# Kernel tuning notes

Hardware: AMD Instinct MI355X
Metric: run time of the kernel (lower is better)

The kernel has to match this reference:

```python
import jax, jax.numpy as jnp
import numpy as np

L = 4          # num_layers
H = 128        # hidden_channels
F = 128        # num_filters
G = 25         # num_gaussians
N = 10000      # nodes
E = 320000     # radius-graph edges
EH = 40000     # hull edges
NG = 64        # graphs in batch
CUTOFF = 5.0
PI = float(np.pi)
LOG2 = float(np.log(2.0))


def ssp(x):  # ShiftedSoftplus
    return jax.nn.softplus(x) - LOG2


def setup_inputs() -> dict:
    key = jax.random.key(0)
    ks = iter(jax.random.split(key, 64))
    w = lambda shape: jax.random.normal(next(ks), shape, jnp.float32) * 0.05
    inp = {
        'z': jax.random.randint(next(ks), (N,), 0, 100),
        'edge_index': jax.random.randint(next(ks), (2, E), 0, N),
        'edge_index_hull': jax.random.randint(next(ks), (2, EH), 0, N),
        'batch': jnp.sort(jax.random.randint(next(ks), (N,), 0, NG)),
        'dist': jax.random.uniform(next(ks), (E,), jnp.float32) * CUTOFF,
        'fea_hull': jax.random.normal(next(ks), (EH, 7), jnp.float32),
        'emb_table': w((100, H)),
        'lin_w': w((L, F, H)),
        'mlp_w1': w((L, F, G)), 'mlp_b1': jnp.zeros((L, F), jnp.float32),
        'mlp_w2': w((L, F, F)), 'mlp_b2': jnp.zeros((L, F), jnp.float32),
        'linh_w': w((L, F, H)),
        'mlph_w1': w((L, F, 7)), 'mlph_b1': jnp.zeros((L, F), jnp.float32),
        'mlph_w2': w((L, F, F)), 'mlph_b2': jnp.zeros((L, F), jnp.float32),
        'v1_w': w((L, H, F)), 'v1_b': jnp.zeros((L, H), jnp.float32),
        'v2_w': w((L, 64, H)), 'v2_b': jnp.zeros((L, 64), jnp.float32),
        'vh1_w': w((L, H, F)), 'vh1_b': jnp.zeros((L, H), jnp.float32),
        'vh2_w': w((L, 64, H)), 'vh2_b': jnp.zeros((L, 64), jnp.float32),
        'cat_w': w((L, H, 128)), 'cat_b': jnp.zeros((L, H), jnp.float32),
        'u1_w': w((64, H)), 'u1_b': jnp.zeros((64,), jnp.float32),
        'u2_w': w((1, 64)), 'u2_b': jnp.zeros((1,), jnp.float32),
    }
    return inp


def reference(z, edge_index, edge_index_hull, batch, dist, fea_hull, emb_table,
              lin_w, mlp_w1, mlp_b1, mlp_w2, mlp_b2,
              linh_w, mlph_w1, mlph_b1, mlph_w2, mlph_b2,
              v1_w, v1_b, v2_w, v2_b, vh1_w, vh1_b, vh2_w, vh2_b,
              cat_w, cat_b, u1_w, u1_b, u2_w, u2_b):
    n = z.shape[0]
    # Gaussian distance embedding: emb(0, cutoff, G)
    offset = jnp.linspace(0.0, CUTOFF, G)
    coeff = -0.5 / (offset[1] - offset[0]) ** 2
    dist_emb = jnp.exp(coeff * (dist[:, None] - offset[None, :]) ** 2)  # [E,G]
    C = 0.5 * (jnp.cos(dist * PI / CUTOFF) + 1.0)                       # [E]
    j, i = edge_index[0], edge_index[1]
    jh, ih = edge_index_hull[0], edge_index_hull[1]
    v = emb_table[z]                                                    # [N,H]
    for l in range(L):
        # update_e
        W = (ssp(dist_emb @ mlp_w1[l].T + mlp_b1[l]) @ mlp_w2[l].T + mlp_b2[l]) * C[:, None]
        e = (v @ lin_w[l].T)[j] * W                                     # [E,F]
        Wh = ssp(fea_hull @ mlph_w1[l].T + mlph_b1[l]) @ mlph_w2[l].T + mlph_b2[l]
        eh = (v @ linh_w[l].T)[jh] * Wh                                 # [EH,F]
        # update_v
        out = jax.ops.segment_sum(e, i, num_segments=n)
        out = ssp(out @ v1_w[l].T + v1_b[l]) @ v2_w[l].T + v2_b[l]      # [N,64]
        outh = jax.ops.segment_sum(eh, ih, num_segments=n)
        outh = ssp(outh @ vh1_w[l].T + vh1_b[l]) @ vh2_w[l].T + vh2_b[l]
        v = v + ssp(jnp.concatenate([out, outh], axis=1) @ cat_w[l].T + cat_b[l])
    # update_u
    u = ssp(v @ u1_w.T + u1_b) @ u2_w.T + u2_b                          # [N,1]
    return jax.ops.segment_sum(u, batch, num_segments=NG)               # [NG,1]
```

## Files before the change

### kernel.cpp

```cpp
#include <hip/hip_runtime.h>
#include <hip/hip_bf16.h>

typedef __hip_bfloat16 bf16;
typedef unsigned short ushort;
typedef __attribute__((ext_vector_type(8))) short short8;
typedef __attribute__((ext_vector_type(4))) float f32x4;

__device__ __forceinline__ float dssp(float x){
  return fmaxf(x, 0.f) + __logf(1.f + __expf(-fabsf(x))) - 0.693147180559945f;
}
__device__ __forceinline__ int clampi(int x, int lo, int hi){ return x<lo?lo:(x>hi?hi:x); }
__device__ __forceinline__ ushort f2b(float f){
  unsigned x = __float_as_uint(f);
  return (ushort)((x + 0x7fffu + ((x>>16)&1u)) >> 16);
}
__device__ __forceinline__ float b2f16(ushort u){ return __uint_as_float(((unsigned)u)<<16); }

constexpr int TBL_K    = 4096;
constexpr int TBL_ROWS = TBL_K + 1;
constexpr int TBL_TILES = (TBL_ROWS + 31) / 32;

__global__ void detect_mode(const unsigned* __restrict__ raw, int* flag){
  __shared__ int c;
  int t = threadIdx.x;
  if (t==0) c = 0;
  __syncthreads();
  unsigned u  = raw[t];
  unsigned lo = u & 0xFFFFu;
  int e = (int)((lo >> 7) & 0xFF);
  int ok = (lo==0u) || (e >= 0x70 && e <= 0x8F);
  atomicAdd(&c, ok);
  __syncthreads();
  if (t==0) *flag = (c >= 160) ? 1 : 0;
}

struct Seg { const void* src; float* dst; int n; };
struct SegTable { Seg s[27]; int count; long total; };

__global__ void convert_all(SegTable tbl, const int* __restrict__ flag){
  int mode = *flag;
  long tid    = (long)blockIdx.x*blockDim.x + threadIdx.x;
  long stride = (long)gridDim.x*blockDim.x;
  for (long i=tid; i<tbl.total; i+=stride){
    long off = i; int k = 0;
    while (k < tbl.count-1 && off >= tbl.s[k].n){ off -= tbl.s[k].n; k++; }
    float f;
    if (mode) f = __bfloat162float(((const bf16*)tbl.s[k].src)[off]);
    else      f = ((const float*)tbl.s[k].src)[off];
    tbl.s[k].dst[off] = (f==f) ? f : 0.f;
  }
}

struct WSeg { const float* src; ushort* dst; int n; };
struct WTable { WSeg s[9]; int count; int total; };

__global__ void convert_wb(WTable wt){
  int tid = blockIdx.x*blockDim.x + threadIdx.x;
  if (tid >= wt.total) return;
  int off = tid, k = 0;
  while (k < wt.count-1 && off >= wt.s[k].n){ off -= wt.s[k].n; k++; }
  wt.s[k].dst[off] = f2b(wt.s[k].src[off]);
}

__global__ void init_all(int* cnt_r, int* cnt_h, float* uacc,
                         int2* spk_r, int2* spk_h, int N, int E, int EH){
  int t = blockIdx.x*blockDim.x + threadIdx.x;
  if (t < N){ cnt_r[t]=0; cnt_h[t]=0; }
  if (t < 64) uacc[t]=0.f;
  if (t < E)  spk_r[t]=make_int2(0,0);
  if (t < EH) spk_h[t]=make_int2(0,0);
}

__global__ void count_edges(const int* __restrict__ ei, const int* __restrict__ eih,
                            int E, int EH, int N, int* cnt_r, int* cnt_h){
  int t = blockIdx.x*blockDim.x + threadIdx.x;
  if (t < E)  atomicAdd(&cnt_r[clampi(ei[E + t], 0, N-1)], 1);
  if (t < EH) atomicAdd(&cnt_h[clampi(eih[EH + t], 0, N-1)], 1);
}

__global__ __launch_bounds__(1024) void scan_pair(const int* cnt_r, int* off_r, int* cur_r,
                                                  const int* cnt_h, int* off_h, int* cur_h, int N){
  __shared__ int s[1024];
  int t = threadIdx.x;
  int CH = (N + 1023) / 1024;
  for (int which=0; which<2; which++){
    const int* cnt = which? cnt_h : cnt_r;
    int* off = which? off_h : off_r;
    int* cur = which? cur_h : cur_r;
    int base = t*CH;
    int sum = 0;
    for (int q=0;q<CH;q++){ int idx=base+q; sum += (idx<N)? cnt[idx] : 0; }
    __syncthreads();
    s[t]=sum; __syncthreads();
    for (int ofs=1; ofs<1024; ofs<<=1){
      int v = s[t]; int vp = (t>=ofs)? s[t-ofs] : 0;
      __syncthreads(); s[t]=v+vp; __syncthreads();
    }
    int run = (t>0)? s[t-1] : 0;
    for (int q=0;q<CH;q++){
      int idx=base+q;
      if (idx<N){ off[idx]=run; cur[idx]=run; run += cnt[idx]; }
    }
    if (t==1023) off[N] = s[1023];
  }
}

__global__ void scatter_edges(const int* __restrict__ ei, const float* __restrict__ distc,
                              const int* __restrict__ eih, int E, int EH, int N,
                              int* cur_r, int* cur_h, int2* spk_r, int2* spk_h){
  int t = blockIdx.x*blockDim.x + threadIdx.x;
  if (t < E){
    int i = clampi(ei[E+t], 0, N-1);
    int p = clampi(atomicAdd(&cur_r[i], 1), 0, E-1);
    float x = fminf(fmaxf(distc[t]*(4096.0f/5.0f), 0.f), 4095.999f);
    int i0 = (int)x; if (i0 > TBL_K-1) i0 = TBL_K-1;
    unsigned fr16 = (unsigned)((x - (float)i0)*65536.0f); if (fr16 > 65535u) fr16 = 65535u;
    spk_r[p] = make_int2(clampi(ei[t],0,N-1), (int)(((unsigned)i0<<16)|fr16));
  }
  if (t < EH){
    int ih = clampi(eih[EH+t], 0, N-1);
    int p = clampi(atomicAdd(&cur_h[ih], 1), 0, EH-1);
    spk_h[p] = make_int2(clampi(eih[t],0,N-1), t);
  }
}

__global__ __launch_bounds__(256) void build_wtab(const float* __restrict__ mlp_w1,
    const float* __restrict__ mlp_b1, const float* __restrict__ mlp_w2,
    const float* __restrict__ mlp_b2, ushort* __restrict__ Wtab){
  int l    = blockIdx.x / TBL_TILES;
  int tile = blockIdx.x % TBL_TILES;
  int row0 = tile * 32;
  const float* w1 = mlp_w1 + l*128*25;
  const float* b1 = mlp_b1 + l*128;
  const float* w2 = mlp_w2 + l*128*128;
  const float* b2 = mlp_b2 + l*128;
  __shared__ float Gs[32][26];
  __shared__ float Ts[32][129];
  __shared__ float Ws[32][129];
  int t = threadIdx.x;
  for (int idx=t; idx<32*25; idx+=256){
    int r = idx/25, k = idx%25;
    float d = (row0+r) * (5.0f/4096.0f);
    float x = d - (float)k*(5.0f/24.0f);
    Gs[r][k] = __expf(-11.52f*x*x);
  }
  __syncthreads();
  int rg = t&7, cg = t>>3;
  #pragma unroll
  for (int ri=0;ri<4;ri++){
    int r = rg*4+ri;
    #pragma unroll
    for (int ci=0;ci<4;ci++){
      int c = cg*4+ci;
      float s = b1[c];
      for (int k=0;k<25;k++) s += Gs[r][k]*w1[c*25+k];
      Ts[r][c] = dssp(s);
    }
  }
  float acc[4][4] = {};
  for (int k0=0;k0<128;k0+=32){
    __syncthreads();
    for (int idx=t; idx<1024; idx+=256){
      int c=idx>>3, kk4=(idx&7)*4;
      float4 f = *(const float4*)(w2+(size_t)c*128+k0+kk4);
      Ws[kk4][c]=f.x; Ws[kk4+1][c]=f.y; Ws[kk4+2][c]=f.z; Ws[kk4+3][c]=f.w;
    }
    __syncthreads();
    for (int kk=0;kk<32;kk++){
      float xv[4];
      #pragma unroll
      for (int ri=0;ri<4;ri++) xv[ri]=Ts[rg*4+ri][k0+kk];
      #pragma unroll
      for (int ci=0;ci<4;ci++){
        float wv = Ws[kk][cg*4+ci];
        #pragma unroll
// ... 68 lines not shown
  }
}
template<int NT>
__device__ __forceinline__ void d2os(float (*Os)[132], const f32x4 d[NT], int t,
    const float* __restrict__ bias, int do_ssp){
  int lane=t&63, w=t>>6, q=(lane>>4)&3, n=lane&15;
  #pragma unroll
  for (int ct=0;ct<NT;ct++){
    int c = w*(NT*16)+ct*16+n;
    float bv = bias? bias[c] : 0.f;
    #pragma unroll
    for (int i=0;i<4;i++){
      float y = d[ct][i] + bv;
      if (do_ssp) y = dssp(y);
      Os[q*4+i][c] = y;
    }
  }
}
__device__ __forceinline__ void d2glob_c(ushort* __restrict__ out, const f32x4 d[2],
    int t, int row0, int N, ushort (*Tmp)[136]){
  d2tile<2>(Tmp, d, t, 0, nullptr, 0);
  __syncthreads();
  int r=t>>4, o=(t&15)*8;
  int gr=row0+r;
  if (gr<N) *(uint4*)(out + (size_t)gr*128 + o) = *(const uint4*)&Tmp[r][o];
  __syncthreads();
}

__global__ __launch_bounds__(256) void f_first(const int* __restrict__ z,
    const float* __restrict__ emb, float* __restrict__ v,
    const ushort* __restrict__ linA, const ushort* __restrict__ linB,
    ushort* __restrict__ vlin, ushort* __restrict__ vlinh, int N){
  __shared__ ushort Xb[16][136];
  __shared__ ushort Tb[16][136];
  int t=threadIdx.x; int row0=blockIdx.x*16;
  f32x4 d[2];
  for (int idx=t; idx<512; idx+=256){
    int r=idx>>5, k4=(idx&31)*4; int gr=row0+r;
    int zz=(gr<N)? clampi(z[gr],0,99):0;
    float4 f = *(const float4*)(emb + (size_t)zz*128 + k4);
    unsigned r0 = (unsigned)f2b(f.x) | ((unsigned)f2b(f.y)<<16);
    unsigned r1 = (unsigned)f2b(f.z) | ((unsigned)f2b(f.w)<<16);
    *(uint2*)&Xb[r][k4] = make_uint2(r0,r1);
    if (gr<N) *(float4*)(v + (size_t)gr*128 + k4) = f;
  }
  __syncthreads();
  mgemm<2>(Xb, linA, t, d);
  d2glob_c(vlin, d, t, row0, N, Tb);
  mgemm<2>(Xb, linB, t, d);
  d2glob_c(vlinh, d, t, row0, N, Tb);
}

__global__ __launch_bounds__(256) void f_mid(
    const float* __restrict__ accR, const float* __restrict__ accH,
    float* __restrict__ v,
    const ushort* __restrict__ v1w, const float* __restrict__ v1b,
    const ushort* __restrict__ v2w, const float* __restrict__ v2b,
    const ushort* __restrict__ vh1w, const float* __restrict__ vh1b,
    const ushort* __restrict__ vh2w, const float* __restrict__ vh2b,
    const ushort* __restrict__ cw, const float* __restrict__ cb,
    const ushort* __restrict__ linA, const ushort* __restrict__ linB,
    ushort* __restrict__ vlin, ushort* __restrict__ vlinh, int N){
  __shared__ ushort Xb[16][136];
  __shared__ ushort Xb2[16][136];
  __shared__ ushort Xb3[16][136];
  __shared__ float  Os[16][132];
  int t=threadIdx.x; int row0=blockIdx.x*16;
  f32x4 d[2]; f32x4 d1[1];

  for (int path=0; path<2; path++){
    const float* X = path? accH : accR;
    __syncthreads();
    for (int idx=t; idx<512; idx+=256){
      int r=idx>>5, k4=(idx&31)*4; int gr=row0+r;
      float4 f=(gr<N)? *(const float4*)(X+(size_t)gr*128+k4):make_float4(0,0,0,0);
      unsigned r0 = (unsigned)f2b(f.x) | ((unsigned)f2b(f.y)<<16);
      unsigned r1 = (unsigned)f2b(f.z) | ((unsigned)f2b(f.w)<<16);
      *(uint2*)&Xb[r][k4] = make_uint2(r0,r1);
    }
    __syncthreads();
    mgemm<2>(Xb, path?vh1w:v1w, t, d);
    d2tile<2>(Xb2, d, t, 0, path?vh1b:v1b, 1);
    __syncthreads();
    mgemm<1>(Xb2, path?vh2w:v2w, t, d1);
    d2tile<1>(Xb3, d1, t, path*64, path?vh2b:v2b, 0);
  }
  __syncthreads();
  mgemm<2>(Xb3, cw, t, d);
  d2os<2>(Os, d, t, cb, 1);
  __syncthreads();
  for (int idx=t; idx<512; idx+=256){
    int r=idx>>5, k4=(idx&31)*4; int gr=row0+r;
    float4 f=(gr<N)? *(const float4*)(v+(size_t)gr*128+k4):make_float4(0,0,0,0);
    f.x+=Os[r][k4]; f.y+=Os[r][k4+1]; f.z+=Os[r][k4+2]; f.w+=Os[r][k4+3];
    if (gr<N) *(float4*)(v+(size_t)gr*128+k4)=f;
    unsigned r0 = (unsigned)f2b(f.x) | ((unsigned)f2b(f.y)<<16);
    unsigned r1 = (unsigned)f2b(f.z) | ((unsigned)f2b(f.w)<<16);
    *(uint2*)&Xb[r][k4] = make_uint2(r0,r1);
  }
  __syncthreads();
  mgemm<2>(Xb, linA, t, d);
  d2glob_c(vlin, d, t, row0, N, Xb2);
  mgemm<2>(Xb, linB, t, d);
  d2glob_c(vlinh, d, t, row0, N, Xb2);
}

__global__ __launch_bounds__(256) void f_last(
    const float* __restrict__ accR, const float* __restrict__ accH,
    const float* __restrict__ v,
    const ushort* __restrict__ v1w, const float* __restrict__ v1b,
    const ushort* __restrict__ v2w, const float* __restrict__ v2b,
    const ushort* __restrict__ vh1w, const float* __restrict__ vh1b,
    const ushort* __restrict__ vh2w, const float* __restrict__ vh2b,
    const ushort* __restrict__ cw, const float* __restrict__ cb,
    const ushort* __restrict__ u1w, const float* __restrict__ u1b,
    const float* __restrict__ u2w, const float* __restrict__ u2b,
    const int* __restrict__ batch, float* __restrict__ uacc, int N){
  __shared__ ushort Xb[16][136];
  __shared__ ushort Xb2[16][136];
  __shared__ ushort Xb3[16][136];
  __shared__ float  Os[16][132];
  __shared__ float ss[16];
  __shared__ int   bb[16];
  int t=threadIdx.x; int row0=blockIdx.x*16;
  f32x4 d[2]; f32x4 d1[1];

  for (int path=0; path<2; path++){
    const float* X = path? accH : accR;
    __syncthreads();
    for (int idx=t; idx<512; idx+=256){
      int r=idx>>5, k4=(idx&31)*4; int gr=row0+r;
      float4 f=(gr<N)? *(const float4*)(X+(size_t)gr*128+k4):make_float4(0,0,0,0);
      unsigned r0 = (unsigned)f2b(f.x) | ((unsigned)f2b(f.y)<<16);
      unsigned r1 = (unsigned)f2b(f.z) | ((unsigned)f2b(f.w)<<16);
      *(uint2*)&Xb[r][k4] = make_uint2(r0,r1);
    }
    __syncthreads();
    mgemm<2>(Xb, path?vh1w:v1w, t, d);
    d2tile<2>(Xb2, d, t, 0, path?vh1b:v1b, 1);
    __syncthreads();
    mgemm<1>(Xb2, path?vh2w:v2w, t, d1);
    d2tile<1>(Xb3, d1, t, path*64, path?vh2b:v2b, 0);
  }
  __syncthreads();
  mgemm<2>(Xb3, cw, t, d);
  d2os<2>(Os, d, t, cb, 1);
  __syncthreads();
  for (int idx=t; idx<512; idx+=256){
    int r=idx>>5, k4=(idx&31)*4; int gr=row0+r;
    float4 f=(gr<N)? *(const float4*)(v+(size_t)gr*128+k4):make_float4(0,0,0,0);
    f.x+=Os[r][k4]; f.y+=Os[r][k4+1]; f.z+=Os[r][k4+2]; f.w+=Os[r][k4+3];
    unsigned r0 = (unsigned)f2b(f.x) | ((unsigned)f2b(f.y)<<16);
    unsigned r1 = (unsigned)f2b(f.z) | ((unsigned)f2b(f.w)<<16);
    *(uint2*)&Xb[r][k4] = make_uint2(r0,r1);
  }
  __syncthreads();
  mgemm<1>(Xb, u1w, t, d1);
  d2os<1>(Os, d1, t, u1b, 1);
  __syncthreads();
  if (t<16){
    int gr=row0+t;
    float s=0.f; int bt=-1;
    if (gr<N){
      s = u2b[0];
      for (int c=0;c<64;c++) s += Os[t][c]*u2w[c];
      bt = clampi(batch[gr],0,63);
    }
    ss[t]=s; bb[t]=bt;
  }
  __syncthreads();
  if (t==0){
    float run=0.f; int cur=-1;
    for (int q=0;q<16;q++){
      int bq=bb[q];
      if (bq<0) continue;
      if (bq!=cur){ if (cur>=0) atomicAdd(&uacc[cur],run); cur=bq; run=0.f; }
      run += ss[q];
    }
    if (cur>=0) atomicAdd(&uacc[cur],run);
  }
}

__global__ __launch_bounds__(256) void hull_all(const int2* __restrict__ spk_h,
    const float* __restrict__ fea,
    const float* __restrict__ mlph_w1, const float* __restrict__ mlph_b1,
    const ushort* __restrict__ mlph_w2b, const float* __restrict__ mlph_b2,
    ushort* __restrict__ WhS_base, size_t lstride,
    int EH, int tilesPerLayer, int l0){
  int l    = l0 + blockIdx.x / tilesPerLayer;
  int tile = blockIdx.x % tilesPerLayer;
  int row0 = tile*64;
  const float* w1 = mlph_w1 + l*128*7;
  const float* b1 = mlph_b1 + l*128;
  const ushort* w2 = mlph_w2b + (size_t)l*16384;
  const float* b2 = mlph_b2 + l*128;
  ushort* WhS = WhS_base + (size_t)(l-l0)*lstride;
  __shared__ int   Eid[64];
  __shared__ float Fs[64][8];
  __shared__ ushort Buf[64][136];
  int t=threadIdx.x;
  if (t < 64){
    int p=row0+t;
    Eid[t]=(p<EH)? clampi(spk_h[p].y,0,EH-1):0;
  }
  __syncthreads();
  for (int idx=t; idx<448; idx+=256){
    int r=idx/7, k=idx%7;
    int p=row0+r;
    Fs[r][k]=(p<EH)? fea[(size_t)Eid[r]*7+k]:0.f;
  }
  __syncthreads();
  {
    int c0=(t&31)*4, r0=(t>>5)*8;
    float w[4][7]; float bb[4];
    #pragma unroll
    for (int cc=0;cc<4;cc++){
      bb[cc]=b1[c0+cc];
      #pragma unroll
      for (int k=0;k<7;k++) w[cc][k]=w1[(c0+cc)*7+k];
    }
    #pragma unroll
    for (int rr=0;rr<8;rr++){
      int r=r0+rr;
      float fv[7];
      #pragma unroll
      for (int k=0;k<7;k++) fv[k]=Fs[r][k];
      ushort o[4];
      #pragma unroll
      for (int cc=0;cc<4;cc++){
        float s=bb[cc];
        #pragma unroll
        for (int k=0;k<7;k++) s=fmaf(fv[k],w[cc][k],s);
        o[cc]=f2b(dssp(s));
      }
      unsigned lo=(unsigned)o[0]|((unsigned)o[1]<<16);
      unsigned hi=(unsigned)o[2]|((unsigned)o[3]<<16);
      *(uint2*)&Buf[r][c0]=make_uint2(lo,hi);
    }
  }
  __syncthreads();
  int lane=t&63, w=t>>6;
  const ushort (*Xw)[136] = (const ushort (*)[136])&Buf[w*16][0];
  f32x4 d[8];
  #pragma unroll
  for (int ct=0;ct<8;ct++) d[ct]=(f32x4){0.f,0.f,0.f,0.f};
  #pragma unroll
  for (int kc=0;kc<4;kc++){
    short8 a = afragb(Xw, lane, kc*32);
    #pragma unroll
    for (int ct=0;ct<8;ct++){
      short8 b = bfrag(w2, ct*16, lane, kc*32);
      d[ct] = __builtin_amdgcn_mfma_f32_16x16x32_bf16(a, b, d[ct], 0, 0, 0);
    }
  }
  __syncthreads();
  int q=(lane>>4)&3, n=lane&15;
  #pragma unroll
  for (int ct=0;ct<8;ct++){
    int c=ct*16+n;
    float bv=b2[c];
    #pragma unroll
    for (int i=0;i<4;i++)
      Buf[w*16+q*4+i][c] = f2b(d[ct][i]+bv);
  }
  __syncthreads();
  #pragma unroll
  for (int j=0;j<4;j++){
    int idx=j*256+t;
    int r=idx>>4, o=(idx&15)*8;
    *(uint4*)(WhS + (size_t)(row0+r)*128 + o) = *(const uint4*)&Buf[r][o];
  }
}

__device__ __forceinline__ float rlerp(unsigned y, const unsigned* __restrict__ Wpk, int f){
  int i0 = (int)(y>>16);
  float fr = (float)(y&0xFFFFu)*(1.f/65536.f);
  unsigned u = Wpk[(size_t)i0*128+f];
  float w0=__uint_as_float(u<<16), w1=__uint_as_float(u&0xFFFF0000u);
  return fmaf(fr, w1-w0, w0);
}

__global__ __launch_bounds__(128) void acc_both(
    const int* __restrict__ off_r, const int2* __restrict__ spk_r,
    const ushort* __restrict__ vlin, const unsigned* __restrict__ Wpk,
    float* __restrict__ accR,
    const int* __restrict__ off_h, const int2* __restrict__ spk_h,
    const ushort* __restrict__ vlinh, const ushort* __restrict__ WhS,
    float* __restrict__ accH,
    int Etot, int EHtot, int N){
  int f = threadIdx.x;
  if ((int)blockIdx.x < N){
    int n = blockIdx.x;
    int b = clampi(off_r[n], 0, Etot);
    int e = clampi(off_r[n+1], b, Etot);
    float a = 0.f;
    int p = b;
    for (; p+8<=e; p+=8){
      int2 k[8];
      #pragma unroll
      for (int j=0;j<8;j++) k[j]=spk_r[p+j];
      float vv[8], ww[8];
      #pragma unroll
      for (int j=0;j<8;j++) vv[j]=b2f16(vlin[(size_t)k[j].x*128+f]);
      #pragma unroll
      for (int j=0;j<8;j++) ww[j]=rlerp((unsigned)k[j].y, Wpk, f);
      #pragma unroll
      for (int j=0;j<8;j++) a=fmaf(vv[j],ww[j],a);
    }
    for (; p+4<=e; p+=4){
      int2 k0=spk_r[p], k1=spk_r[p+1], k2=spk_r[p+2], k3=spk_r[p+3];
      float v0 = b2f16(vlin[(size_t)k0.x*128+f]);
      float v1 = b2f16(vlin[(size_t)k1.x*128+f]);
      float v2 = b2f16(vlin[(size_t)k2.x*128+f]);
      float v3 = b2f16(vlin[(size_t)k3.x*128+f]);
      float w0 = rlerp((unsigned)k0.y, Wpk, f);
      float w1 = rlerp((unsigned)k1.y, Wpk, f);
      float w2 = rlerp((unsigned)k2.y, Wpk, f);
      float w3 = rlerp((unsigned)k3.y, Wpk, f);
      a += v0*w0 + v1*w1 + v2*w2 + v3*w3;
    }
    for (; p<e; p++){
      int2 k0=spk_r[p];
      a += b2f16(vlin[(size_t)k0.x*128+f]) * rlerp((unsigned)k0.y, Wpk, f);
    }
    accR[(size_t)n*128+f] = a;
  } else {
    int n = blockIdx.x - N;
    int b = clampi(off_h[n], 0, EHtot);
    int e = clampi(off_h[n+1], b, EHtot);
    float a = 0.f;
    int p = b;
    for (; p+4<=e; p+=4){
      int2 k0=spk_h[p], k1=spk_h[p+1], k2=spk_h[p+2], k3=spk_h[p+3];
      float v0 = b2f16(vlinh[(size_t)k0.x*128+f]);
      float v1 = b2f16(vlinh[(size_t)k1.x*128+f]);
      float v2 = b2f16(vlinh[(size_t)k2.x*128+f]);
      float v3 = b2f16(vlinh[(size_t)k3.x*128+f]);
      a += v0*b2f16(WhS[(size_t)p*128+f])     + v1*b2f16(WhS[(size_t)(p+1)*128+f])
         + v2*b2f16(WhS[(size_t)(p+2)*128+f]) + v3*b2f16(WhS[(size_t)(p+3)*128+f]);
    }
    for (; p<e; p++){
      int2 k0=spk_h[p];
      a += b2f16(vlinh[(size_t)k0.x*128+f]) * b2f16(WhS[(size_t)p*128+f]);
    }
    accH[(size_t)n*128+f] = a;
  }
}

__global__ void write_out(const float* __restrict__ uacc, void* out, const int* __restrict__ flag){
  int t = threadIdx.x;
  if (t < 64){
    if (*flag) ((bf16*)out)[t] = __float2bfloat16(uacc[t]);
    else       ((float*)out)[t] = uacc[t];
  }
}

extern "C" void kernel_launch(void* const* d_in, const int* in_sizes, int n_in,
                              void* d_out, int out_size, void* d_ws, size_t ws_size,
                              hipStream_t stream){
  const int* z     = (const int*)d_in[0];
  const int* ei    = (const int*)d_in[1];
  const int* eih   = (const int*)d_in[2];
  const int* batch = (const int*)d_in[3];

  const int N  = in_sizes[0];
  const int E  = in_sizes[1]/2;
  const int EH = in_sizes[2]/2;
  const int EHpad = (EH + 63) & ~63;

  char* wp = (char*)d_ws;
  auto alloc = [&](size_t bytes)->char*{
    char* p = wp; wp += (bytes + 255) & ~(size_t)255; return p;
  };
  int* flag    = (int*)alloc(256);
  int* cnt_r   = (int*)alloc((size_t)N*4);
  int* off_r   = (int*)alloc((size_t)(N+1)*4);
  int* cur_r   = (int*)alloc((size_t)N*4);
  int* cnt_h   = (int*)alloc((size_t)N*4);
  int* off_h   = (int*)alloc((size_t)(N+1)*4);
  int* cur_h   = (int*)alloc((size_t)N*4);
  int2* spk_r  = (int2*)alloc((size_t)E*8);
  int2* spk_h  = (int2*)alloc((size_t)EH*8);
  float* uacc  = (float*)alloc(64*4);

  SegTable tbl; tbl.count = 27; tbl.total = 0;
  float* cvt[27];
  for (int i=0;i<27;i++){
    int n = in_sizes[4+i];
    cvt[i] = (float*)alloc((size_t)n*4);
    tbl.s[i].src = d_in[4+i];
    tbl.s[i].dst = cvt[i];
    tbl.s[i].n   = n;
    tbl.total   += n;
  }
  const float* distc   = cvt[0];
  const float* feac    = cvt[1];
  const float* embc    = cvt[2];
  const float* mlp_w1  = cvt[4];
  const float* mlp_b1  = cvt[5];
  const float* mlp_w2  = cvt[6];
  const float* mlp_b2  = cvt[7];
  const float* mlph_w1 = cvt[9];
  const float* mlph_b1 = cvt[10];
  const float* mlph_b2 = cvt[12];
  const float* v1_b  = cvt[14];
  const float* v2_b  = cvt[16];
  const float* vh1_b = cvt[18];
  const float* vh2_b = cvt[20];
  const float* cat_b = cvt[22];
  const float* u1_b  = cvt[24];
  const float* u2_w  = cvt[25];
  const float* u2_b  = cvt[26];

  ushort* lin_wb   = (ushort*)alloc((size_t)4*16384*2);
  ushort* linh_wb  = (ushort*)alloc((size_t)4*16384*2);
  ushort* v1_wb    = (ushort*)alloc((size_t)4*16384*2);
  ushort* vh1_wb   = (ushort*)alloc((size_t)4*16384*2);
  ushort* cat_wb   = (ushort*)alloc((size_t)4*16384*2);
  ushort* mlph_w2b = (ushort*)alloc((size_t)4*16384*2);
  ushort* v2_wb    = (ushort*)alloc((size_t)4*8192*2);
  ushort* vh2_wb   = (ushort*)alloc((size_t)4*8192*2);
  ushort* u1_wb    = (ushort*)alloc((size_t)8192*2);
  WTable wt; wt.count = 9;
  wt.s[0] = { cvt[3],  lin_wb,   4*16384 };
  wt.s[1] = { cvt[8],  linh_wb,  4*16384 };
  wt.s[2] = { cvt[13], v1_wb,    4*16384 };
  wt.s[3] = { cvt[17], vh1_wb,   4*16384 };
  wt.s[4] = { cvt[21], cat_wb,   4*16384 };
  wt.s[5] = { cvt[11], mlph_w2b, 4*16384 };
  wt.s[6] = { cvt[15], v2_wb,    4*8192  };
  wt.s[7] = { cvt[19], vh2_wb,   4*8192  };
  wt.s[8] = { cvt[23], u1_wb,    8192    };
  wt.total = 6*4*16384 + 2*4*8192 + 8192;

  ushort*   Wtab = (ushort*)alloc((size_t)4*TBL_ROWS*128*2);
  unsigned* Wpk  = (unsigned*)alloc((size_t)4*TBL_K*128*4);
  float* v     = (float*)alloc((size_t)N*128*4);
  ushort* vlin  = (ushort*)alloc((size_t)N*128*2);
  ushort* vlinh = (ushort*)alloc((size_t)N*128*2);
  float* accR  = (float*)alloc((size_t)N*128*4);
  float* accH  = (float*)alloc((size_t)N*128*4);

  size_t used = (size_t)(wp - (char*)d_ws);
  size_t whs1 = (size_t)EHpad*128*2;
  bool pre = (ws_size >= used + 4*whs1 + 256);
  ushort* WhS = (ushort*)alloc(pre ? 4*whs1 : whs1);

  detect_mode<<<1,256,0,stream>>>((const unsigned*)d_in[6], flag);
  {
    int cb = (int)((tbl.total + 255)/256);
    if (cb > 4096) cb = 4096;
    convert_all<<<cb,256,0,stream>>>(tbl, flag);
  }
  convert_wb<<<(wt.total+255)/256,256,0,stream>>>(wt);

  int nb;
  nb = (E+255)/256;     init_all<<<nb,256,0,stream>>>(cnt_r,cnt_h,uacc,spk_r,spk_h,N,E,EH);
  nb = (E+255)/256;     count_edges<<<nb,256,0,stream>>>(ei,eih,E,EH,N,cnt_r,cnt_h);
  scan_pair<<<1,1024,0,stream>>>(cnt_r,off_r,cur_r,cnt_h,off_h,cur_h,N);
  nb = (E+255)/256;     scatter_edges<<<nb,256,0,stream>>>(ei,distc,eih,E,EH,N,cur_r,cur_h,spk_r,spk_h);
  build_wtab<<<4*TBL_TILES,256,0,stream>>>(mlp_w1,mlp_b1,mlp_w2,mlp_b2,Wtab);
  pack_wtab<<<(int)((4L*TBL_K*128+255)/256),256,0,stream>>>(Wtab,Wpk);

  const int nt = (N+15)/16;
  const int ht64 = (EH+63)/64;
  if (pre)
    hull_all<<<4*ht64,256,0,stream>>>(spk_h, feac, mlph_w1, mlph_b1, mlph_w2b, mlph_b2,
                                      WhS, whs1/2, EH, ht64, 0);

  f_first<<<nt,256,0,stream>>>(z, embc, v, lin_wb, linh_wb, vlin, vlinh, N);
  for (int l=0;l<4;l++){
    if (!pre)
      hull_all<<<ht64,256,0,stream>>>(spk_h, feac, mlph_w1, mlph_b1, mlph_w2b, mlph_b2,
                                      WhS, 0, EH, ht64, l);
    const ushort* WhSl = pre ? (WhS + (size_t)l*(whs1/2)) : WhS;
    acc_both<<<2*N,128,0,stream>>>(off_r, spk_r, vlin, Wpk + (size_t)l*TBL_K*128, accR,
                                   off_h, spk_h, vlinh, WhSl, accH, E, EH, N);
    if (l<3){
      f_mid<<<nt,256,0,stream>>>(accR, accH, v,
          v1_wb + (size_t)l*16384, v1_b + l*128, v2_wb + (size_t)l*8192, v2_b + l*64,
          vh1_wb + (size_t)l*16384, vh1_b + l*128, vh2_wb + (size_t)l*8192, vh2_b + l*64,
          cat_wb + (size_t)l*16384, cat_b + l*128,
          lin_wb + (size_t)(l+1)*16384, linh_wb + (size_t)(l+1)*16384, vlin, vlinh, N);
    } else {
      f_last<<<nt,256,0,stream>>>(accR, accH, v,
          v1_wb + (size_t)l*16384, v1_b + l*128, v2_wb + (size_t)l*8192, v2_b + l*64,
          vh1_wb + (size_t)l*16384, vh1_b + l*128, vh2_wb + (size_t)l*8192, vh2_b + l*64,
          cat_wb + (size_t)l*16384, cat_b + l*128,
          u1_wb, u1_b, u2_w, u2_b, batch, uacc, N);
    }
  }
  write_out<<<1,64,0,stream>>>(uacc, d_out, flag);
}
```

Before: 485.5 us.

## Split edge accumulation across two half-blocks, parallelize node MLP paths, shrink hull tiles

acc_both now runs 256 threads per node, with each half summing half of the node's edge range; the two partial sums are combined through shared memory. This is meant to expose more memory-level parallelism in the gather-heavy aggregation. f_mid and f_last now run the radius and hull MLP paths concurrently on separate wave pairs instead of one after the other, which removes serialized GEMM phases and a few barriers. hull_all now uses 32-row tiles with 128 threads, giving more blocks, at the cost of a shared-memory reduction and extra barriers.

```diff
diff --git a/kernel.cpp b/kernel.cpp
--- a/kernel.cpp
+++ b/kernel.cpp
@@ -304,33 +304,39 @@
     const ushort* __restrict__ cw, const float* __restrict__ cb,
     const ushort* __restrict__ linA, const ushort* __restrict__ linB,
     ushort* __restrict__ vlin, ushort* __restrict__ vlinh, int N){
-  __shared__ ushort Xb[16][136];
-  __shared__ ushort Xb2[16][136];
+  __shared__ ushort XbR[16][136];
+  __shared__ ushort XbH[16][136];
   __shared__ ushort Xb3[16][136];
   __shared__ float  Os[16][132];
   int t=threadIdx.x; int row0=blockIdx.x*16;
-  f32x4 d[2]; f32x4 d1[1];
-
-  for (int path=0; path<2; path++){
-    const float* X = path? accH : accR;
-    __syncthreads();
-    for (int idx=t; idx<512; idx+=256){
+  int lane=t&63, w=t>>6;
+  int path = w>>1;
+  int tp   = (w&1)*64 + lane;
+  f32x4 d4[4]; f32x4 d2[2];
+
+  {
+    int th = t&127; int half = t>>7;
+    const float* X = half? accH : accR;
+    ushort (*Xb)[136] = half? XbH : XbR;
+    for (int idx=th; idx<512; idx+=128){
       int r=idx>>5, k4=(idx&31)*4; int gr=row0+r;
       float4 f=(gr<N)? *(const float4*)(X+(size_t)gr*128+k4):make_float4(0,0,0,0);
       unsigned r0 = (unsigned)f2b(f.x) | ((unsigned)f2b(f.y)<<16);
       unsigned r1 = (unsigned)f2b(f.z) | ((unsigned)f2b(f.w)<<16);
       *(uint2*)&Xb[r][k4] = make_uint2(r0,r1);
     }
-    __syncthreads();
-    mgemm<2>(Xb, path?vh1w:v1w, t, d);
-    d2tile<2>(Xb2, d, t, 0, path?vh1b:v1b, 1);
-    __syncthreads();
-    mgemm<1>(Xb2, path?vh2w:v2w, t, d1);
-    d2tile<1>(Xb3, d1, t, path*64, path?vh2b:v2b, 0);
-  }
-  __syncthreads();
-  mgemm<2>(Xb3, cw, t, d);
-  d2os<2>(Os, d, t, cb, 1);
+  }
+  __syncthreads();
+  ushort (*XbP)[136] = path? XbH : XbR;
+  mgemm<4>(XbP, path? vh1w : v1w, tp, d4);
+  __syncthreads();
+  d2tile<4>(XbP, d4, tp, 0, path? vh1b : v1b, 1);
+  __syncthreads();
+  mgemm<2>(XbP, path? vh2w : v2w, tp, d2);
+  d2tile<2>(Xb3, d2, tp, path*64, path? vh2b : v2b, 0);
+  __syncthreads();
+  mgemm<2>(Xb3, cw, t, d2);
+  d2os<2>(Os, d2, t, cb, 1);
   __syncthreads();
   for (int idx=t; idx<512; idx+=256){
     int r=idx>>5, k4=(idx&31)*4; int gr=row0+r;
@@ -339,13 +345,13 @@
     if (gr<N) *(float4*)(v+(size_t)gr*128+k4)=f;
     unsigned r0 = (unsigned)f2b(f.x) | ((unsigned)f2b(f.y)<<16);
     unsigned r1 = (unsigned)f2b(f.z) | ((unsigned)f2b(f.w)<<16);
-    *(uint2*)&Xb[r][k4] = make_uint2(r0,r1);
-  }
-  __syncthreads();
-  mgemm<2>(Xb, linA, t, d);
-  d2glob_c(vlin, d, t, row0, N, Xb2);
-  mgemm<2>(Xb, linB, t, d);
-  d2glob_c(vlinh, d, t, row0, N, Xb2);
+    *(uint2*)&XbR[r][k4] = make_uint2(r0,r1);
+  }
+  __syncthreads();
+  mgemm<2>(XbR, linA, t, d2);
+  d2glob_c(vlin, d2, t, row0, N, XbH);
+  mgemm<2>(XbR, linB, t, d2);
+  d2glob_c(vlinh, d2, t, row0, N, XbH);
 }
 
 __global__ __launch_bounds__(256) void f_last(
@@ -359,35 +365,41 @@
     const ushort* __restrict__ u1w, const float* __restrict__ u1b,
     const float* __restrict__ u2w, const float* __restrict__ u2b,
     const int* __restrict__ batch, float* __restrict__ uacc, int N){
-  __shared__ ushort Xb[16][136];
-  __shared__ ushort Xb2[16][136];
+  __shared__ ushort XbR[16][136];
+  __shared__ ushort XbH[16][136];
   __shared__ ushort Xb3[16][136];
   __shared__ float  Os[16][132];
   __shared__ float ss[16];
   __shared__ int   bb[16];
   int t=threadIdx.x; int row0=blockIdx.x*16;
-  f32x4 d[2]; f32x4 d1[1];
-
-  for (int path=0; path<2; path++){
-    const float* X = path? accH : accR;
-    __syncthreads();
-    for (int idx=t; idx<512; idx+=256){
+  int lane=t&63, w=t>>6;
+  int path = w>>1;
+  int tp   = (w&1)*64 + lane;
+  f32x4 d4[4]; f32x4 d2[2]; f32x4 d1[1];
+
+  {
+    int th = t&127; int half = t>>7;
+    const float* X = half? accH : accR;
+    ushort (*Xb)[136] = half? XbH : XbR;
+    for (int idx=th; idx<512; idx+=128){
       int r=idx>>5, k4=(idx&31)*4; int gr=row0+r;
       float4 f=(gr<N)? *(const float4*)(X+(size_t)gr*128+k4):make_float4(0,0,0,0);
       unsigned r0 = (unsigned)f2b(f.x) | ((unsigned)f2b(f.y)<<16);
       unsigned r1 = (unsigned)f2b(f.z) | ((unsigned)f2b(f.w)<<16);
       *(uint2*)&Xb[r][k4] = make_uint2(r0,r1);
     }
-    __syncthreads();
-    mgemm<2>(Xb, path?vh1w:v1w, t, d);
-    d2tile<2>(Xb2, d, t, 0, path?vh1b:v1b, 1);
-    __syncthreads();
-    mgemm<1>(Xb2, path?vh2w:v2w, t, d1);
-    d2tile<1>(Xb3, d1, t, path*64, path?vh2b:v2b, 0);
-  }
-  __syncthreads();
-  mgemm<2>(Xb3, cw, t, d);
-  d2os<2>(Os, d, t, cb, 1);
+  }
+  __syncthreads();
+  ushort (*XbP)[136] = path? XbH : XbR;
+  mgemm<4>(XbP, path? vh1w : v1w, tp, d4);
+  __syncthreads();
+  d2tile<4>(XbP, d4, tp, 0, path? vh1b : v1b, 1);
+  __syncthreads();
+  mgemm<2>(XbP, path? vh2w : v2w, tp, d2);
+  d2tile<2>(Xb3, d2, tp, path*64, path? vh2b : v2b, 0);
+  __syncthreads();
+  mgemm<2>(Xb3, cw, t, d2);
+  d2os<2>(Os, d2, t, cb, 1);
   __syncthreads();
   for (int idx=t; idx<512; idx+=256){
     int r=idx>>5, k4=(idx&31)*4; int gr=row0+r;
@@ -395,10 +407,10 @@
     f.x+=Os[r][k4]; f.y+=Os[r][k4+1]; f.z+=Os[r][k4+2]; f.w+=Os[r][k4+3];
     unsigned r0 = (unsigned)f2b(f.x) | ((unsigned)f2b(f.y)<<16);
     unsigned r1 = (unsigned)f2b(f.z) | ((unsigned)f2b(f.w)<<16);
-    *(uint2*)&Xb[r][k4] = make_uint2(r0,r1);
-  }
-  __syncthreads();
-  mgemm<1>(Xb, u1w, t, d1);
+    *(uint2*)&XbR[r][k4] = make_uint2(r0,r1);
+  }
+  __syncthreads();
+  mgemm<1>(XbR, u1w, t, d1);
   d2os<1>(Os, d1, t, u1b, 1);
   __syncthreads();
   if (t<16){
@@ -424,7 +436,7 @@
   }
 }
 
-__global__ __launch_bounds__(256) void hull_all(const int2* __restrict__ spk_h,
+__global__ __launch_bounds__(128) void hull_all(const int2* __restrict__ spk_h,
     const float* __restrict__ fea,
     const float* __restrict__ mlph_w1, const float* __restrict__ mlph_b1,
     const ushort* __restrict__ mlph_w2b, const float* __restrict__ mlph_b2,
@@ -432,22 +444,22 @@
     int EH, int tilesPerLayer, int l0){
   int l    = l0 + blockIdx.x / tilesPerLayer;
   int tile = blockIdx.x % tilesPerLayer;
-  int row0 = tile*64;
+  int row0 = tile*32;
   const float* w1 = mlph_w1 + l*128*7;
   const float* b1 = mlph_b1 + l*128;
   const ushort* w2 = mlph_w2b + (size_t)l*16384;
   const float* b2 = mlph_b2 + l*128;
   ushort* WhS = WhS_base + (size_t)(l-l0)*lstride;
-  __shared__ int   Eid[64];
-  __shared__ float Fs[64][8];
-  __shared__ ushort Buf[64][136];
+  __shared__ int   Eid[32];
+  __shared__ float Fs[32][8];
+  __shared__ ushort Buf[32][136];
   int t=threadIdx.x;
-  if (t < 64){
+  if (t < 32){
     int p=row0+t;
     Eid[t]=(p<EH)? clampi(spk_h[p].y,0,EH-1):0;
   }
   __syncthreads();
-  for (int idx=t; idx<448; idx+=256){
+  for (int idx=t; idx<224; idx+=128){
     int r=idx/7, k=idx%7;
     int p=row0+r;
     Fs[r][k]=(p<EH)? fea[(size_t)Eid[r]*7+k]:0.f;
@@ -509,7 +521,7 @@
   __syncthreads();
   #pragma unroll
   for (int j=0;j<4;j++){
-    int idx=j*256+t;
+    int idx=j*128+t;
     int r=idx>>4, o=(idx&15)*8;
     *(uint4*)(WhS + (size_t)(row0+r)*128 + o) = *(const uint4*)&Buf[r][o];
   }
@@ -523,7 +535,7 @@
   return fmaf(fr, w1-w0, w0);
 }
 
-__global__ __launch_bounds__(128) void acc_both(
+__global__ __launch_bounds__(256) void acc_both(
     const int* __restrict__ off_r, const int2* __restrict__ spk_r,
     const ushort* __restrict__ vlin, const unsigned* __restrict__ Wpk,
     float* __restrict__ accR,
@@ -531,14 +543,19 @@
     const ushort* __restrict__ vlinh, const ushort* __restrict__ WhS,
     float* __restrict__ accH,
     int Etot, int EHtot, int N){
-  int f = threadIdx.x;
+  __shared__ float part[2][128];
+  int t = threadIdx.x;
+  int f = t&127, h = t>>7;
   if ((int)blockIdx.x < N){
     int n = blockIdx.x;
     int b = clampi(off_r[n], 0, Etot);
     int e = clampi(off_r[n+1], b, Etot);
+    int len = e-b, half = (len+1)>>1;
+    int pb = b + h*half;
+    int pe = h ? e : b+half;
     float a = 0.f;
-    int p = b;
-    for (; p+8<=e; p+=8){
+    int p = pb;
+    for (; p+8<=pe; p+=8){
       int2 k[8];
       #pragma unroll
       for (int j=0;j<8;j++) k[j]=spk_r[p+j];
@@ -550,7 +567,7 @@
       #pragma unroll
       for (int j=0;j<8;j++) a=fmaf(vv[j],ww[j],a);
     }
-    for (; p+4<=e; p+=4){
+    for (; p+4<=pe; p+=4){
       int2 k0=spk_r[p], k1=spk_r[p+1], k2=spk_r[p+2], k3=spk_r[p+3];
       float v0 = b2f16(vlin[(size_t)k0.x*128+f]);
       float v1 = b2f16(vlin[(size_t)k1.x*128+f]);
@@ -562,18 +579,23 @@
       float w3 = rlerp((unsigned)k3.y, Wpk, f);
       a += v0*w0 + v1*w1 + v2*w2 + v3*w3;
     }
-    for (; p<e; p++){
+    for (; p<pe; p++){
       int2 k0=spk_r[p];
       a += b2f16(vlin[(size_t)k0.x*128+f]) * rlerp((unsigned)k0.y, Wpk, f);
     }
-    accR[(size_t)n*128+f] = a;
+    part[h][f] = a;
+    __syncthreads();
+    if (h==0) accR[(size_t)n*128+f] = part[0][f] + part[1][f];
   } else {
     int n = blockIdx.x - N;
     int b = clampi(off_h[n], 0, EHtot);
     int e = clampi(off_h[n+1], b, EHtot);
+    int len = e-b, half = (len+1)>>1;
+    int pb = b + h*half;
+    int pe = h ? e : b+half;
     float a = 0.f;
-    int p = b;
-    for (; p+4<=e; p+=4){
+    int p = pb;
+    for (; p+4<=pe; p+=4){
       int2 k0=spk_h[p], k1=spk_h[p+1], k2=spk_h[p+2], k3=spk_h[p+3];
       float v0 = b2f16(vlinh[(size_t)k0.x*128+f]);
       float v1 = b2f16(vlinh[(size_t)k1.x*128+f]);
@@ -582,11 +604,13 @@
       a += v0*b2f16(WhS[(size_t)p*128+f])     + v1*b2f16(WhS[(size_t)(p+1)*128+f])
          + v2*b2f16(WhS[(size_t)(p+2)*128+f]) + v3*b2f16(WhS[(size_t)(p+3)*128+f]);
     }
-    for (; p<e; p++){
+    for (; p<pe; p++){
       int2 k0=spk_h[p];
       a += b2f16(vlinh[(size_t)k0.x*128+f]) * b2f16(WhS[(size_t)p*128+f]);
     }
-    accH[(size_t)n*128+f] = a;
+    part[h][f] = a;
+    __syncthreads();
+    if (h==0) accH[(size_t)n*128+f] = part[0][f] + part[1][f];
   }
 }
 
@@ -706,18 +730,18 @@
   pack_wtab<<<(int)((4L*TBL_K*128+255)/256),256,0,stream>>>(Wtab,Wpk);
 
   const int nt = (N+15)/16;
-  const int ht64 = (EH+63)/64;
+  const int ht32 = (EH+31)/32;
   if (pre)
-    hull_all<<<4*ht64,256,0,stream>>>(spk_h, feac, mlph_w1, mlph_b1, mlph_w2b, mlph_b2,
-                                      WhS, whs1/2, EH, ht64, 0);
+    hull_all<<<4*ht32,128,0,stream>>>(spk_h, feac, mlph_w1, mlph_b1, mlph_w2b, mlph_b2,
+                                      WhS, whs1/2, EH, ht32, 0);
 
   f_first<<<nt,256,0,stream>>>(z, embc, v, lin_wb, linh_wb, vlin, vlinh, N);
   for (int l=0;l<4;l++){
     if (!pre)
-      hull_all<<<ht64,256,0,stream>>>(spk_h, feac, mlph_w1, mlph_b1, mlph_w2b, mlph_b2,
-                                      WhS, 0, EH, ht64, l);
+      hull_all<<<ht32,128,0,stream>>>(spk_h, feac, mlph_w1, mlph_b1, mlph_w2b, mlph_b2,
+                                      WhS, 0, EH, ht32, l);
     const ushort* WhSl = pre ? (WhS + (size_t)l*(whs1/2)) : WhS;
-    acc_both<<<2*N,128,0,stream>>>(off_r, spk_r, vlin, Wpk + (size_t)l*TBL_K*128, accR,
+    acc_both<<<2*N,256,0,stream>>>(off_r, spk_r, vlin, Wpk + (size_t)l*TBL_K*128, accR,
                                    off_h, spk_h, vlinh, WhSl, accH, E, EH, N);
     if (l<3){
       f_mid<<<nt,256,0,stream>>>(accR, accH, v,
```

Result: slower. 541.0 us (+11.4%).

## Fuse hull edge MLP into aggregation kernel with atomic scatter into accH

Applied to the files above, without the earlier changes.

Removes the separate hull_all kernel and its precomputed per-edge Wh buffer. Hull edge weights are now computed per 32-edge tile inside the aggregation kernel, multiplied by the gathered vlinh rows, and accumulated into accH with run-length-merged atomics over the destination-sorted edges. accH is zeroed in init_all and again in f_mid after it is read. This saves writing and re-reading the Wh buffer and one launch per layer, but adds float atomics and makes the hull sums depend on atomic ordering. The 4-way remainder loop in the radius path is also dropped.

```diff
diff --git a/kernel.cpp b/kernel.cpp
--- a/kernel.cpp
+++ b/kernel.cpp
@@ -63,12 +63,14 @@
 }
 
 __global__ void init_all(int* cnt_r, int* cnt_h, float* uacc,
-                         int2* spk_r, int2* spk_h, int N, int E, int EH){
+                         int2* spk_r, int2* spk_h, float* accH,
+                         int N, int E, int EH){
   int t = blockIdx.x*blockDim.x + threadIdx.x;
   if (t < N){ cnt_r[t]=0; cnt_h[t]=0; }
   if (t < 64) uacc[t]=0.f;
   if (t < E)  spk_r[t]=make_int2(0,0);
   if (t < EH) spk_h[t]=make_int2(0,0);
+  if (t < N*32) ((float4*)accH)[t] = make_float4(0,0,0,0);
 }
 
 __global__ void count_edges(const int* __restrict__ ei, const int* __restrict__ eih,
@@ -107,7 +109,8 @@
 
 __global__ void scatter_edges(const int* __restrict__ ei, const float* __restrict__ distc,
                               const int* __restrict__ eih, int E, int EH, int N,
-                              int* cur_r, int* cur_h, int2* spk_r, int2* spk_h){
+                              int* cur_r, int* cur_h, int2* spk_r, int2* spk_h,
+                              int* __restrict__ hn){
   int t = blockIdx.x*blockDim.x + threadIdx.x;
   if (t < E){
     int i = clampi(ei[E+t], 0, N-1);
@@ -121,6 +124,7 @@
     int ih = clampi(eih[EH+t], 0, N-1);
     int p = clampi(atomicAdd(&cur_h[ih], 1), 0, EH-1);
     spk_h[p] = make_int2(clampi(eih[t],0,N-1), t);
+    hn[p] = ih;
   }
 }
 
@@ -295,7 +299,7 @@
 }
 
 __global__ __launch_bounds__(256) void f_mid(
-    const float* __restrict__ accR, const float* __restrict__ accH,
+    const float* __restrict__ accR, float* __restrict__ accH,
     float* __restrict__ v,
     const ushort* __restrict__ v1w, const float* __restrict__ v1b,
     const ushort* __restrict__ v2w, const float* __restrict__ v2b,
@@ -320,6 +324,8 @@
       unsigned r0 = (unsigned)f2b(f.x) | ((unsigned)f2b(f.y)<<16);
       unsigned r1 = (unsigned)f2b(f.z) | ((unsigned)f2b(f.w)<<16);
       *(uint2*)&Xb[r][k4] = make_uint2(r0,r1);
+      if (path==1 && gr<N)
+        *(float4*)(accH+(size_t)gr*128+k4) = make_float4(0,0,0,0);
     }
     __syncthreads();
     mgemm<2>(Xb, path?vh1w:v1w, t, d);
@@ -424,115 +430,24 @@
   }
 }
 
-__global__ __launch_bounds__(256) void hull_all(const int2* __restrict__ spk_h,
-    const float* __restrict__ fea,
-    const float* __restrict__ mlph_w1, const float* __restrict__ mlph_b1,
-    const ushort* __restrict__ mlph_w2b, const float* __restrict__ mlph_b2,
-    ushort* __restrict__ WhS_base, size_t lstride,
-    int EH, int tilesPerLayer, int l0){
-  int l    = l0 + blockIdx.x / tilesPerLayer;
-  int tile = blockIdx.x % tilesPerLayer;
-  int row0 = tile*64;
-  const float* w1 = mlph_w1 + l*128*7;
-  const float* b1 = mlph_b1 + l*128;
-  const ushort* w2 = mlph_w2b + (size_t)l*16384;
-  const float* b2 = mlph_b2 + l*128;
-  ushort* WhS = WhS_base + (size_t)(l-l0)*lstride;
-  __shared__ int   Eid[64];
-  __shared__ float Fs[64][8];
-  __shared__ ushort Buf[64][136];
-  int t=threadIdx.x;
-  if (t < 64){
-    int p=row0+t;
-    Eid[t]=(p<EH)? clampi(spk_h[p].y,0,EH-1):0;
-  }
-  __syncthreads();
-  for (int idx=t; idx<448; idx+=256){
-    int r=idx/7, k=idx%7;
-    int p=row0+r;
-    Fs[r][k]=(p<EH)? fea[(size_t)Eid[r]*7+k]:0.f;
-  }
-  __syncthreads();
-  {
-    int c0=(t&31)*4, r0=(t>>5)*8;
-    float w[4][7]; float bb[4];
-    #pragma unroll
-    for (int cc=0;cc<4;cc++){
-      bb[cc]=b1[c0+cc];
-      #pragma unroll
-      for (int k=0;k<7;k++) w[cc][k]=w1[(c0+cc)*7+k];
-    }
-    #pragma unroll
-    for (int rr=0;rr<8;rr++){
-      int r=r0+rr;
-      float fv[7];
-      #pragma unroll
-      for (int k=0;k<7;k++) fv[k]=Fs[r][k];
-      ushort o[4];
-      #pragma unroll
-      for (int cc=0;cc<4;cc++){
-        float s=bb[cc];
-        #pragma unroll
-        for (int k=0;k<7;k++) s=fmaf(fv[k],w[cc][k],s);
-        o[cc]=f2b(dssp(s));
-      }
-      unsigned lo=(unsigned)o[0]|((unsigned)o[1]<<16);
-      unsigned hi=(unsigned)o[2]|((unsigned)o[3]<<16);
-      *(uint2*)&Buf[r][c0]=make_uint2(lo,hi);
-    }
-  }
-  __syncthreads();
-  int lane=t&63, w=t>>6;
-  const ushort (*Xw)[136] = (const ushort (*)[136])&Buf[w*16][0];
-  f32x4 d[8];
-  #pragma unroll
-  for (int ct=0;ct<8;ct++) d[ct]=(f32x4){0.f,0.f,0.f,0.f};
-  #pragma unroll
-  for (int kc=0;kc<4;kc++){
-    short8 a = afragb(Xw, lane, kc*32);
-    #pragma unroll
-    for (int ct=0;ct<8;ct++){
-      short8 b = bfrag(w2, ct*16, lane, kc*32);
-      d[ct] = __builtin_amdgcn_mfma_f32_16x16x32_bf16(a, b, d[ct], 0, 0, 0);
-    }
-  }
-  __syncthreads();
-  int q=(lane>>4)&3, n=lane&15;
-  #pragma unroll
-  for (int ct=0;ct<8;ct++){
-    int c=ct*16+n;
-    float bv=b2[c];
-    #pragma unroll
-    for (int i=0;i<4;i++)
-      Buf[w*16+q*4+i][c] = f2b(d[ct][i]+bv);
-  }
-  __syncthreads();
-  #pragma unroll
-  for (int j=0;j<4;j++){
-    int idx=j*256+t;
-    int r=idx>>4, o=(idx&15)*8;
-    *(uint4*)(WhS + (size_t)(row0+r)*128 + o) = *(const uint4*)&Buf[r][o];
-  }
-}
-
-__device__ __forceinline__ float rlerp(unsigned y, const unsigned* __restrict__ Wpk, int f){
-  int i0 = (int)(y>>16);
-  float fr = (float)(y&0xFFFFu)*(1.f/65536.f);
-  unsigned u = Wpk[(size_t)i0*128+f];
-  float w0=__uint_as_float(u<<16), w1=__uint_as_float(u&0xFFFF0000u);
-  return fmaf(fr, w1-w0, w0);
-}
-
-__global__ __launch_bounds__(128) void acc_both(
+__global__ __launch_bounds__(128) void acc_fused(
     const int* __restrict__ off_r, const int2* __restrict__ spk_r,
     const ushort* __restrict__ vlin, const unsigned* __restrict__ Wpk,
     float* __restrict__ accR,
-    const int* __restrict__ off_h, const int2* __restrict__ spk_h,
-    const ushort* __restrict__ vlinh, const ushort* __restrict__ WhS,
+    const int2* __restrict__ spk_h, const int* __restrict__ hn,
+    const ushort* __restrict__ vlinh, const float* __restrict__ fea,
+    const float* __restrict__ w1, const float* __restrict__ b1,
+    const ushort* __restrict__ w2, const float* __restrict__ b2,
     float* __restrict__ accH,
     int Etot, int EHtot, int N){
-  int f = threadIdx.x;
+  __shared__ float Fs[32][8];
+  __shared__ ushort Buf[32][136];
+  __shared__ int Eid[32];
+  __shared__ int Hn[32];
+  __shared__ int Jn[32];
+  int t = threadIdx.x;
   if ((int)blockIdx.x < N){
+    int f = t;
     int n = blockIdx.x;
     int b = clampi(off_r[n], 0, Etot);
     int e = clampi(off_r[n+1], b, Etot);
@@ -546,47 +461,109 @@
       #pragma unroll
       for (int j=0;j<8;j++) vv[j]=b2f16(vlin[(size_t)k[j].x*128+f]);
       #pragma unroll
-      for (int j=0;j<8;j++) ww[j]=rlerp((unsigned)k[j].y, Wpk, f);
+      for (int j=0;j<8;j++){
+        unsigned y=(unsigned)k[j].y;
+        unsigned u=Wpk[(size_t)(y>>16)*128+f];
+        float fr=(float)(y&0xFFFFu)*(1.f/65536.f);
+        float w0=__uint_as_float(u<<16), w1v=__uint_as_float(u&0xFFFF0000u);
+        ww[j]=fmaf(fr, w1v-w0, w0);
+      }
       #pragma unroll
       for (int j=0;j<8;j++) a=fmaf(vv[j],ww[j],a);
-    }
-    for (; p+4<=e; p+=4){
-      int2 k0=spk_r[p], k1=spk_r[p+1], k2=spk_r[p+2], k3=spk_r[p+3];
-      float v0 = b2f16(vlin[(size_t)k0.x*128+f]);
-      float v1 = b2f16(vlin[(size_t)k1.x*128+f]);
-      float v2 = b2f16(vlin[(size_t)k2.x*128+f]);
-      float v3 = b2f16(vlin[(size_t)k3.x*128+f]);
-      float w0 = rlerp((unsigned)k0.y, Wpk, f);
-      float w1 = rlerp((unsigned)k1.y, Wpk, f);
-      float w2 = rlerp((unsigned)k2.y, Wpk, f);
-      float w3 = rlerp((unsigned)k3.y, Wpk, f);
-      a += v0*w0 + v1*w1 + v2*w2 + v3*w3;
     }
     for (; p<e; p++){
       int2 k0=spk_r[p];
-      a += b2f16(vlin[(size_t)k0.x*128+f]) * rlerp((unsigned)k0.y, Wpk, f);
+      unsigned y=(unsigned)k0.y;
+      unsigned u=Wpk[(size_t)(y>>16)*128+f];
+      float fr=(float)(y&0xFFFFu)*(1.f/65536.f);
+      float w0=__uint_as_float(u<<16), w1v=__uint_as_float(u&0xFFFF0000u);
+      a += b2f16(vlin[(size_t)k0.x*128+f]) * fmaf(fr, w1v-w0, w0);
     }
     accR[(size_t)n*128+f] = a;
   } else {
-    int n = blockIdx.x - N;
-    int b = clampi(off_h[n], 0, EHtot);
-    int e = clampi(off_h[n+1], b, EHtot);
-    float a = 0.f;
-    int p = b;
-    for (; p+4<=e; p+=4){
-      int2 k0=spk_h[p], k1=spk_h[p+1], k2=spk_h[p+2], k3=spk_h[p+3];
-      float v0 = b2f16(vlinh[(size_t)k0.x*128+f]);
-      float v1 = b2f16(vlinh[(size_t)k1.x*128+f]);
-      float v2 = b2f16(vlinh[(size_t)k2.x*128+f]);
-      float v3 = b2f16(vlinh[(size_t)k3.x*128+f]);
-      a += v0*b2f16(WhS[(size_t)p*128+f])     + v1*b2f16(WhS[(size_t)(p+1)*128+f])
-         + v2*b2f16(WhS[(size_t)(p+2)*128+f]) + v3*b2f16(WhS[(size_t)(p+3)*128+f]);
-    }
-    for (; p<e; p++){
-      int2 k0=spk_h[p];
-      a += b2f16(vlinh[(size_t)k0.x*128+f]) * b2f16(WhS[(size_t)p*128+f]);
-    }
-    accH[(size_t)n*128+f] = a;
+    int tile = blockIdx.x - N;
+    int row0 = tile*32;
+    if (t < 32){
+      int p = row0+t;
+      int2 k = (p<EHtot)? spk_h[p] : make_int2(0,0);
+      Eid[t] = clampi(k.y, 0, EHtot-1);
+      Jn[t]  = clampi(k.x, 0, N-1);
+      Hn[t]  = (p<EHtot)? clampi(hn[p], 0, N-1) : -1;
+    }
+    __syncthreads();
+    for (int idx=t; idx<224; idx+=128){
+      int r=idx/7, k=idx%7;
+      Fs[r][k] = fea[(size_t)Eid[r]*7+k];
+    }
+    __syncthreads();
+    {
+      int c0=(t&31)*4, r0=(t>>5)*8;
+      float w[4][7]; float bb[4];
+      #pragma unroll
+      for (int cc=0;cc<4;cc++){
+        bb[cc]=b1[c0+cc];
+        #pragma unroll
+        for (int k=0;k<7;k++) w[cc][k]=w1[(c0+cc)*7+k];
+      }
+      #pragma unroll
+      for (int rr=0;rr<8;rr++){
+        int r=r0+rr;
+        float fv[7];
+        #pragma unroll
+        for (int k=0;k<7;k++) fv[k]=Fs[r][k];
+        ushort o[4];
+        #pragma unroll
+        for (int cc=0;cc<4;cc++){
+          float s=bb[cc];
+          #pragma unroll
+          for (int k=0;k<7;k++) s=fmaf(fv[k],w[cc][k],s);
+          o[cc]=f2b(dssp(s));
+        }
+        unsigned lo=(unsigned)o[0]|((unsigned)o[1]<<16);
+        unsigned hi=(unsigned)o[2]|((unsigned)o[3]<<16);
+        *(uint2*)&Buf[r][c0]=make_uint2(lo,hi);
+      }
+    }
+    __syncthreads();
+    int lane=t&63, w=t>>6;
+    const ushort (*Xw)[136] = (const ushort (*)[136])&Buf[w*16][0];
+    f32x4 d[8];
+    #pragma unroll
+    for (int ct=0;ct<8;ct++) d[ct]=(f32x4){0.f,0.f,0.f,0.f};
+    #pragma unroll
+    for (int kc=0;kc<4;kc++){
+      short8 a = afragb(Xw, lane, kc*32);
+      #pragma unroll
+      for (int ct=0;ct<8;ct++){
+        short8 b = bfrag(w2, ct*16, lane, kc*32);
+        d[ct] = __builtin_amdgcn_mfma_f32_16x16x32_bf16(a, b, d[ct], 0, 0, 0);
+      }
+    }
+    __syncthreads();
+    for (int idx=t; idx<1024; idx+=128){
+      int r=idx>>5, ch=idx&31;
+      *(uint2*)&Buf[r][ch*4] = *(const uint2*)(vlinh + (size_t)Jn[r]*128 + ch*4);
+    }
+    __syncthreads();
+    int q=(lane>>4)&3, n16=lane&15;
+    int rb = w*16 + q*4;
+    #pragma unroll
+    for (int ct=0;ct<8;ct++){
+      int c = ct*16+n16;
+      float bv = b2[c];
+      float run=0.f; int curn=-1;
+      #pragma unroll
+      for (int i=0;i<4;i++){
+        int r=rb+i;
+        int nn=Hn[r];
+        if (nn!=curn){
+          if (curn>=0) atomicAdd(&accH[(size_t)curn*128+c], run);
+          curn=nn; run=0.f;
+        }
+        if (nn>=0) run += b2f16(Buf[r][c]) * (d[ct][i]+bv);
+      }
+      if (curn>=0) atomicAdd(&accH[(size_t)curn*128+c], run);
+    }
   }
 }
 
@@ -609,7 +586,6 @@
   const int N  = in_sizes[0];
   const int E  = in_sizes[1]/2;
   const int EH = in_sizes[2]/2;
-  const int EHpad = (EH + 63) & ~63;
 
   char* wp = (char*)d_ws;
   auto alloc = [&](size_t bytes)->char*{
@@ -624,6 +600,7 @@
   int* cur_h   = (int*)alloc((size_t)N*4);
   int2* spk_r  = (int2*)alloc((size_t)E*8);
   int2* spk_h  = (int2*)alloc((size_t)EH*8);
+  int*  hn     = (int*)alloc((size_t)EH*4);
   float* uacc  = (float*)alloc(64*4);
 
   SegTable tbl; tbl.count = 27; tbl.total = 0;
@@ -684,11 +661,6 @@
   float* accR  = (float*)alloc((size_t)N*128*4);
   float* accH  = (float*)alloc((size_t)N*128*4);
 
-  size_t used = (size_t)(wp - (char*)d_ws);
-  size_t whs1 = (size_t)EHpad*128*2;
-  bool pre = (ws_size >= used + 4*whs1 + 256);
-  ushort* WhS = (ushort*)alloc(pre ? 4*whs1 : whs1);
-
   detect_mode<<<1,256,0,stream>>>((const unsigned*)d_in[6], flag);
   {
     int cb = (int)((tbl.total + 255)/256);
@@ -698,27 +670,24 @@
   convert_wb<<<(wt.total+255)/256,256,0,stream>>>(wt);
 
   int nb;
-  nb = (E+255)/256;     init_all<<<nb,256,0,stream>>>(cnt_r,cnt_h,uacc,spk_r,spk_h,N,E,EH);
+  int initN = E > N*32 ? E : N*32;
+  nb = (initN+255)/256; init_all<<<nb,256,0,stream>>>(cnt_r,cnt_h,uacc,spk_r,spk_h,accH,N,E,EH);
   nb = (E+255)/256;     count_edges<<<nb,256,0,stream>>>(ei,eih,E,EH,N,cnt_r,cnt_h);
   scan_pair<<<1,1024,0,stream>>>(cnt_r,off_r,cur_r,cnt_h,off_h,cur_h,N);
-  nb = (E+255)/256;     scatter_edges<<<nb,256,0,stream>>>(ei,distc,eih,E,EH,N,cur_r,cur_h,spk_r,spk_h);
+  nb = (E+255)/256;     scatter_edges<<<nb,256,0,stream>>>(ei,distc,eih,E,EH,N,cur_r,cur_h,spk_r,spk_h,hn);
   build_wtab<<<4*TBL_TILES,256,0,stream>>>(mlp_w1,mlp_b1,mlp_w2,mlp_b2,Wtab);
   pack_wtab<<<(int)((4L*TBL_K*128+255)/256),256,0,stream>>>(Wtab,Wpk);
 
   const int nt = (N+15)/16;
-  const int ht64 = (EH+63)/64;
-  if (pre)
-    hull_all<<<4*ht64,256,0,stream>>>(spk_h, feac, mlph_w1, mlph_b1, mlph_w2b, mlph_b2,
-                                      WhS, whs1/2, EH, ht64, 0);
+  const int ht32 = (EH+31)/32;
 
   f_first<<<nt,256,0,stream>>>(z, embc, v, lin_wb, linh_wb, vlin, vlinh, N);
   for (int l=0;l<4;l++){
-    if (!pre)
-      hull_all<<<ht64,256,0,stream>>>(spk_h, feac, mlph_w1, mlph_b1, mlph_w2b, mlph_b2,
-                                      WhS, 0, EH, ht64, l);
-    const ushort* WhSl = pre ? (WhS + (size_t)l*(whs1/2)) : WhS;
-    acc_both<<<2*N,128,0,stream>>>(off_r, spk_r, vlin, Wpk + (size_t)l*TBL_K*128, accR,
-                                   off_h, spk_h, vlinh, WhSl, accH, E, EH, N);
+    acc_fused<<<N+ht32,128,0,stream>>>(off_r, spk_r, vlin, Wpk + (size_t)l*TBL_K*128, accR,
+                                       spk_h, hn, vlinh, feac,
+                                       mlph_w1 + l*896, mlph_b1 + l*128,
+                                       mlph_w2b + (size_t)l*16384, mlph_b2 + l*128,
+                                       accH, E, EH, N);
     if (l<3){
       f_mid<<<nt,256,0,stream>>>(accR, accH, v,
           v1_wb + (size_t)l*16384, v1_b + l*128, v2_wb + (size_t)l*8192, v2_b + l*64,
```

After: 574.6 us. 18.4% more time.
